# Kernel tuning notes

Hardware: AMD Instinct MI355X
Metric: run time of the kernel (lower is better)

## Reference

```python
import jax, jax.numpy as jnp
import numpy as np

DIM = 256
NH = 8
HGT = 32
WID = 32
B = 8


def rel_indices(S):
    # (1, S*S, S*S, 3) with channels (dx, dy, d^2), matching torch construction
    ind = jnp.arange(S)[None, :] - jnp.arange(S)[:, None]          # (S,S)
    indx = jnp.tile(ind, (S, S))                                    # (S^2,S^2)
    indy = jnp.repeat(jnp.repeat(ind, S, axis=0), S, axis=1)        # (S^2,S^2)
    indd = indx ** 2 + indy ** 2
    return jnp.stack([indx, indy, indd], axis=-1).astype(jnp.float32)[None]


def setup_inputs() -> dict:
    key = jax.random.key(0)
    ks = jax.random.split(key, 8)
    std = 0.02
    x = jax.random.normal(ks[0], (B, DIM, HGT, WID), dtype=jnp.float32)
    input_mask = jnp.ones((B, HGT, WID), dtype=jnp.float32)
    Wqk = jax.random.normal(ks[1], (2 * DIM, DIM), dtype=jnp.float32) * std  # qkv_bias=False
    Wv = jax.random.normal(ks[2], (DIM, DIM), dtype=jnp.float32) * std
    Wproj = jax.random.normal(ks[3], (DIM, DIM), dtype=jnp.float32) * std
    bproj = jnp.zeros((DIM,), dtype=jnp.float32)
    Wpos = jax.random.normal(ks[4], (NH, 3), dtype=jnp.float32) * std
    bpos = jnp.zeros((NH,), dtype=jnp.float32)
    gating = jnp.ones((NH,), dtype=jnp.float32)
    return {"x": x, "input_mask": input_mask, "Wqk": Wqk, "Wv": Wv,
            "Wproj": Wproj, "bproj": bproj, "Wpos": Wpos, "bpos": bpos,
            "gating": gating}


def gpsa_forward(x, input_mask, Wqk, Wv, Wproj, bproj, Wpos, bpos, gating):
    Bq, C, H, W = x.shape
    N = H * W
    nh = gating.shape[0]
    hd = C // nh
    scale = hd ** (-0.5)

    xf = x.reshape(Bq, C, N).transpose(0, 2, 1)          # (B,N,C)
    m = input_mask.reshape(Bq, N)                        # (B,N)

    qk = (xf @ Wqk.T).reshape(Bq, N, 2, nh, hd)
    q = qk[:, :, 0].transpose(0, 2, 1, 3)                # (B,nh,N,hd)
    k = qk[:, :, 1].transpose(0, 2, 1, 3)

    patch_score = jax.nn.softmax(
        jnp.einsum('bhnd,bhmd->bhnm', q, k) * scale, axis=-1)

    rel = rel_indices(H)                                  # (1,N,N,3)
    pos_score = jnp.einsum('unmt,ht->uhnm', rel, Wpos) + bpos[None, :, None, None]
    pos_score = jax.nn.softmax(pos_score, axis=-1)        # (1,nh,N,N)

    g = jax.nn.sigmoid(gating)[None, :, None, None]
    attn = (1.0 - g) * patch_score + g * pos_score
    attn = attn / attn.sum(axis=-1, keepdims=True)
    attn = attn * m[:, None, None, :]                     # mask keys
    attn = attn / attn.sum(axis=-1, keepdims=True)

    v = (xf @ Wv.T).reshape(Bq, N, nh, hd).transpose(0, 2, 1, 3)  # (B,nh,N,hd)
    out = jnp.einsum('bhnm,bhmd->bhnd', attn, v)          # (B,nh,N,hd)
    out = out.transpose(0, 2, 1, 3).reshape(Bq, N, C)
    out = out @ Wproj.T + bproj
    return out.transpose(0, 2, 1).reshape(Bq, C, H, W)


def reference(x, input_mask, Wqk, Wv, Wproj, bproj, Wpos, bpos, gating):
    return gpsa_forward(x, input_mask, Wqk, Wv, Wproj, bproj, Wpos, bpos, gating)
```

## Files before the change

kernel.cpp:

```cpp
#include <hip/hip_runtime.h>
#include <hip/hip_bf16.h>
#include <math.h>

#define B_ 8
#define C_ 256
#define N_ 1024
#define NH_ 8
#define HD_ 32

typedef __attribute__((ext_vector_type(8))) short bf16x8;
typedef __attribute__((ext_vector_type(4))) short bf16x4;
typedef __attribute__((ext_vector_type(4))) float f32x4;
typedef __attribute__((ext_vector_type(16))) float f32x16;
typedef __attribute__((ext_vector_type(2))) unsigned int u32x2;
typedef __attribute__((ext_vector_type(4))) unsigned int u32x4;
#define MFMA16(a,b,c) __builtin_amdgcn_mfma_f32_16x16x32_bf16((a),(b),(c),0,0,0)
#define MFMA32(a,b,c) __builtin_amdgcn_mfma_f32_32x32x16_bf16((a),(b),(c),0,0,0)

static __device__ __forceinline__ short f2bf(float f) {
    __hip_bfloat16 h = __float2bfloat16(f);
    return *reinterpret_cast<short*>(&h);
}
static __device__ __forceinline__ unsigned int cvtpk(float a, float b) {
    unsigned int r;
    asm("v_cvt_pk_bf16_f32 %0, %1, %2" : "=v"(r) : "v"(a), "v"(b));
    return r;
}

#define FS 0.2550352584f

static constexpr size_t OFF_VB   = 0;
static constexpr size_t OFF_QBF  = 8388608;
static constexpr size_t OFF_KFR  = 12582912;
static constexpr size_t OFF_VFR  = 16777216;
static constexpr size_t OFF_E1   = 20971520;
static constexpr size_t OFF_E2   = 21004288;
static constexpr size_t OFF_SE1  = 21037056;
static constexpr size_t OFF_SE2  = 21038080;
static constexpr size_t OFF_A2   = 21039104;
static constexpr size_t A2S      = 36;
static constexpr size_t OFF_O    = 30476288;
static constexpr size_t OFF_WBF  = 34670592;
static constexpr size_t OFF_WPBF = 35063808;
static constexpr size_t OFF_ZFR  = 35194880;

__global__ __launch_bounds__(256) void k_prep(
    const float* __restrict__ Wqk, const float* __restrict__ Wv,
    const float* __restrict__ Wp, const float* __restrict__ mask,
    const float* __restrict__ Wpos, const float* __restrict__ bpos,
    const float* __restrict__ x,
    __hip_bfloat16* __restrict__ wfm, __hip_bfloat16* __restrict__ wpfm,
    __hip_bfloat16* __restrict__ zfrag, __hip_bfloat16* __restrict__ xfm,
    float* __restrict__ e1, float* __restrict__ e2,
    float* __restrict__ se1, float* __restrict__ se2)
{
    const int bx = blockIdx.x;
    const int tid = threadIdx.x;
    __shared__ float ps[2][32][8];
    __shared__ float tile[64][68];
    if (bx < 256) {
        int idx = bx * 256 + tid;
        int row = idx >> 6;
        int c4  = (idx & 63) * 4;
        const float* src = (row < 512) ? (Wqk + (size_t)row*256)
                         : (row < 768) ? (Wv + (size_t)(row-512)*256)
                                       : (Wp + (size_t)(row-768)*256);
        float4 v = *(const float4*)(src + c4);
        bf16x4 pk;
        pk[0] = f2bf(v.x); pk[1] = f2bf(v.y); pk[2] = f2bf(v.z); pk[3] = f2bf(v.w);
        int r2 = (row < 768) ? row : (row - 768);
        __hip_bfloat16* dst = (row < 768) ? wfm : wpfm;
        size_t addr = (size_t)(r2 >> 4)*4096 + (size_t)(c4 >> 5)*512
                    + (size_t)((((c4 >> 3) & 3)*16) + (r2 & 15))*8 + (c4 & 7);
        *(bf16x4*)(dst + addr) = pk;
    } else if (bx < 384) {
        int idx = (bx - 256) * 256 + tid;
        int L8  = idx & 127;
        int mt  = (idx >> 7) & 31;
        int b   = idx >> 12;
        int region = L8 >> 6;
        int slot   = L8 & 63;
        int zrow = slot & 31, shi = slot >> 5;
        bf16x8 v;
        if (zrow == 0) {
            int m = mt*32 + region*16 + shi*8;
            const float* mp = mask + (size_t)b*N_ + m;
            #pragma unroll
            for (int j = 0; j < 8; ++j) v[j] = f2bf(mp[j]);
        } else {
            short c = (zrow == 1) ? (short)0x3F80 : (short)0;
            #pragma unroll
            for (int j = 0; j < 8; ++j) v[j] = c;
        }
        *(bf16x8*)(zfrag + ((size_t)b*32 + mt)*1024 + region*512 + slot*8) = v;
    } else if (bx < 392) {
        const int h = bx - 384;
        const int i = tid >> 3, j4 = (tid & 7) * 4;
        const float wx = Wpos[h*3+0], wy = Wpos[h*3+1], wd = Wpos[h*3+2], bp = bpos[h];
        float fmx = -1e30f, gmx = -1e30f;
        for (int jp = 0; jp < 32; ++jp) {
            float dx = (float)(jp - i);
            float q2 = wd*dx*dx;
            fmx = fmaxf(fmx, wx*dx + q2 + bp);
            gmx = fmaxf(gmx, wy*dx + q2);
        }
        float s1 = 0.f, s2 = 0.f;
        #pragma unroll
        for (int jj = 0; jj < 4; ++jj) {
            int j = j4 + jj;
            float dx = (float)(j - i);
            float q2 = wd*dx*dx;
            float fv = __expf(wx*dx + q2 + bp - fmx);
            float gv = __expf(wy*dx + q2 - gmx);
            e1[h*1024 + i*32 + j] = fv;
            e2[h*1024 + i*32 + j] = gv;
            s1 += fv; s2 += gv;
        }
        ps[0][i][tid & 7] = s1;
        ps[1][i][tid & 7] = s2;
        __syncthreads();
        if (tid < 32) {
            float a = 0.f, c = 0.f;
            #pragma unroll
            for (int k = 0; k < 8; ++k) { a += ps[0][tid][k]; c += ps[1][tid][k]; }
            se1[h*32 + tid] = a;
            se2[h*32 + tid] = c;
        }
    } else {
        const int bx2 = bx - 392;
        const int n0 = (bx2 & 15) * 64, c0 = ((bx2 >> 4) & 3) * 64, b = bx2 >> 6;
        {
            int cl = tid >> 2, nq = (tid & 3) * 16;
            const float* src = x + ((size_t)b*C_ + c0 + cl)*N_ + n0 + nq;
            #pragma unroll
            for (int i = 0; i < 4; ++i)
                *(float4*)&tile[cl][nq + i*4] = ((const float4*)src)[i];
        }
        __syncthreads();
        {
            int nl = tid >> 2, cq = (tid & 3) * 16;
            short pk[16];
            #pragma unroll
            for (int i = 0; i < 16; ++i) pk[i] = f2bf(tile[cq + i][nl]);
            int cg = c0 + cq;
            int ks = cg >> 5, g0 = (cg >> 3) & 3;
            size_t base = ((size_t)b*64 + (n0 >> 4) + (nl >> 4))*4096
                        + (size_t)ks*512 + (size_t)(g0*16 + (nl & 15))*8;
            *(uint4*)(xfm + base)       = *(uint4*)&pk[0];
            *(uint4*)(xfm + base + 128) = *(uint4*)&pk[8];
        }
    }
}

__global__ __launch_bounds__(256) void k_qkv_mfma(
    const __hip_bfloat16* __restrict__ xfm, const __hip_bfloat16* __restrict__ wfm,
    const float* __restrict__ mask,
    __hip_bfloat16* __restrict__ qbf, __hip_bfloat16* __restrict__ kfrag,
    __hip_bfloat16* __restrict__ vfrag, float* __restrict__ vbuf)
{
    const int t = threadIdx.x, w = t >> 6, L = t & 63, lo = L & 15, g = L >> 4;
    const int jw = blockIdx.x * 64 + w * 16;
    const int n0 = blockIdx.y * 64, b = blockIdx.z;

    const __hip_bfloat16* afm = wfm + (size_t)(jw >> 4)*4096 + (size_t)L*8;
    bf16x8 af[8];
    #pragma unroll
    for (int ks = 0; ks < 8; ++ks) af[ks] = *(const bf16x8*)(afm + ks*512);

    const f32x4 Z = {0.f,0.f,0.f,0.f};
    f32x4 D0 = Z, D1 = Z, D2 = Z, D3 = Z;
    const __hip_bfloat16* xb = xfm + ((size_t)b*64 + (n0 >> 4))*4096 + (size_t)L*8;
    #pragma unroll
    for (int ks = 0; ks < 8; ++ks) {
        bf16x8 b0 = *(const bf16x8*)(xb + ks*512);
        bf16x8 b1 = *(const bf16x8*)(xb + 4096 + ks*512);
        bf16x8 b2 = *(const bf16x8*)(xb + 8192 + ks*512);
        bf16x8 b3 = *(const bf16x8*)(xb + 12288 + ks*512);
        D0 = MFMA16(af[ks], b0, D0);
        D1 = MFMA16(af[ks], b1, D1);
        D2 = MFMA16(af[ks], b2, D2);
        D3 = MFMA16(af[ks], b3, D3);
    }
    f32x4 D[4] = {D0, D1, D2, D3};

    const size_t bb = (size_t)b*NH_;
    if (jw < 256) {
        int h = jw >> 5, d0 = (jw & 31) + 4*g;
        #pragma unroll
        for (int nt = 0; nt < 4; ++nt) {
            int nn = n0 + nt*16 + lo;
            bf16x4 pk;
            #pragma unroll
            for (int r = 0; r < 4; ++r) pk[r] = f2bf(D[nt][r] * FS);
            *(bf16x4*)(qbf + ((bb + h)*N_ + nn)*HD_ + d0) = pk;
        }
    } else if (jw < 512) {
        int j2 = jw & 255, h = j2 >> 5, d0 = (j2 & 31) + 4*g;
        size_t base = (bb + h)*32768 + (size_t)(d0 >> 4)*512
                    + (size_t)((d0 >> 3) & 1)*256 + (d0 & 7);
        #pragma unroll
        for (int nt = 0; nt < 4; ++nt) {
            int nn = n0 + nt*16 + lo;
            bf16x4 pk;
            #pragma unroll
            for (int r = 0; r < 4; ++r) pk[r] = f2bf(D[nt][r]);
            *(bf16x4*)(kfrag + base + (size_t)(nn >> 5)*1024 + (nn & 31)*8) = pk;
        }
    } else {
        int j2 = jw - 512, h = j2 >> 5, d0 = (j2 & 31) + 4*g;
        #pragma unroll
        for (int nt = 0; nt < 4; ++nt) {
            int nn = n0 + nt*16 + lo;
            float mval = mask[(size_t)b*N_ + nn];
            float4 fv = make_float4(D[nt][0], D[nt][1], D[nt][2], D[nt][3]);
            *(float4*)(vbuf + ((bb + h)*N_ + nn)*HD_ + d0) = fv;
            size_t vbase = (bb + h)*32768 + (size_t)(nn >> 5)*1024
                         + (size_t)((nn >> 4) & 1)*512 + (size_t)((nn >> 3) & 1)*256
                         + (nn & 7);
            #pragma unroll
            for (int r = 0; r < 4; ++r)
                vfrag[vbase + (size_t)(d0 + r)*8] = __float2bfloat16(D[nt][r] * mval);
        }
    }
}

__global__ __launch_bounds__(256) void k_pos_apply(
    const float* __restrict__ vb, const float* __restrict__ mask,
    const float* __restrict__ e1, const float* __restrict__ e2,
    float* __restrict__ a2)
{
    const int rn = blockIdx.x, h = blockIdx.y, b = blockIdx.z;
    const int tid = threadIdx.x;
    const int cm = tid >> 3, dq = tid & 7;
    __shared__ float t1[32][36];
    __shared__ float e1s[32][36];
    __shared__ float t1m[32];
    __shared__ float e2s[32];
    const float* vbh = vb + (((size_t)b*NH_ + h)*N_)*HD_;
    const float* mb  = mask + (size_t)b*N_;

    {
        int r = tid >> 3, c4 = (tid & 7) * 4;
        *(float4*)&e1s[r][c4] = *(const float4*)(e1 + h*1024 + r*32 + c4);
        if (tid < 32) e2s[tid] = e2[h*1024 + rn*32 + tid];
    }
    __syncthreads();

    {
        float4 acc = make_float4(0.f,0.f,0.f,0.f);
        const float* vcol = vbh + cm*HD_ + dq*4;
        #pragma unroll 8
        for (int rm = 0; rm < 32; ++rm) {
            float4 vv = *(const float4*)(vcol + (size_t)rm*32*HD_);
            float wgt = e2s[rm];
            acc.x = fmaf(wgt, vv.x, acc.x);
            acc.y = fmaf(wgt, vv.y, acc.y);
            acc.z = fmaf(wgt, vv.z, acc.z);
            acc.w = fmaf(wgt, vv.w, acc.w);
        }
        *(float4*)&t1[cm][dq*4] = acc;
    }
    if (tid < 32) {
        float s = 0.f;
        for (int rm = 0; rm < 32; ++rm)
            s = fmaf(e2s[rm], mb[rm*32 + tid], s);
        t1m[tid] = s;
    }
    __syncthreads();

    const size_t bh = (size_t)b*NH_ + h;
    {
        const int cn = cm;
        float4 acc = make_float4(0.f,0.f,0.f,0.f);
        #pragma unroll 8
        for (int ci = 0; ci < 32; ++ci) {
            float wgt = e1s[cn][ci];
            float4 tv = *(const float4*)&t1[ci][dq*4];
            acc.x = fmaf(wgt, tv.x, acc.x);
            acc.y = fmaf(wgt, tv.y, acc.y);
            acc.z = fmaf(wgt, tv.z, acc.z);
            acc.w = fmaf(wgt, tv.w, acc.w);
        }
        int n = rn*32 + cn;
        *(float4*)(a2 + (bh*N_ + n)*A2S + dq*4) = acc;
    }
    if (tid < 32) {
        float s = 0.f;
        for (int ci = 0; ci < 32; ++ci)
            s = fmaf(e1s[tid][ci], t1m[ci], s);
        a2[(bh*N_ + rn*32 + tid)*A2S + 32] = s;
    }
}

__global__ __launch_bounds__(512, 4) void k_attn_mfma(
    const __hip_bfloat16* __restrict__ qbf, const __hip_bfloat16* __restrict__ kfrag,
    const __hip_bfloat16* __restrict__ vfrag, const __hip_bfloat16* __restrict__ zfrag,
    const float* __restrict__ a2, const float* __restrict__ se1,
    const float* __restrict__ se2, const float* __restrict__ gating,
    __hip_bfloat16* __restrict__ ob)
{
    const int bid = blockIdx.x;
    const int swz = ((bid & 7) << 6) | (bid >> 3);
    const int xt = swz & 7, h = (swz >> 3) & 7, b = swz >> 6;

    const int t = threadIdx.x, w = t >> 6, L = t & 63;
    const int ln = L & 31, hi = L >> 5;
    const int nh = w & 3, sp = w >> 2;
    const int n0 = xt * 128 + nh * 32;
    const size_t bh = (size_t)b*NH_ + h;
    const __hip_bfloat16* qh = qbf + bh*(size_t)N_*HD_;
    const size_t spo = (size_t)sp * 16 * 1024;
    const __hip_bfloat16* kf = kfrag + bh*32768 + spo + (size_t)L*8;
    const __hip_bfloat16* vf = vfrag + bh*32768 + spo + (size_t)L*8;
    const __hip_bfloat16* zf = zfrag + (size_t)b*32768 + spo + (size_t)L*8;

    __shared__ float ldsO[128*32];
    __shared__ float ldsZ[128*2];

    bf16x8 qf0 = *(const bf16x8*)(qh + (size_t)(n0 + ln)*HD_ + 8*hi);
    bf16x8 qf1 = *(const bf16x8*)(qh + (size_t)(n0 + ln)*HD_ + 16 + 8*hi);

    f32x16 O; f32x16 Zc;
    #pragma unroll
    for (int i = 0; i < 16; ++i) { O[i] = 0.f; Zc[i] = 0.f; }

    bf16x8 ka0 = *(const bf16x8*)(kf);
    bf16x8 ka1 = *(const bf16x8*)(kf + 512);
    bf16x8 vf0 = *(const bf16x8*)(vf);
    bf16x8 vf1 = *(const bf16x8*)(vf + 512);
    bf16x8 zf0 = *(const bf16x8*)(zf);
    bf16x8 zf1 = *(const bf16x8*)(zf + 512);

    for (int mt = 0; mt < 16; ++mt) {
        f32x16 S;
        #pragma unroll
        for (int i = 0; i < 16; ++i) S[i] = 0.f;
        S = MFMA32(ka0, qf0, S);
        S = MFMA32(ka1, qf1, S);

        const size_t o1 = (size_t)(mt < 15 ? mt + 1 : mt) * 1024;
        bf16x8 nka0 = *(const bf16x8*)(kf + o1);
        bf16x8 nka1 = *(const bf16x8*)(kf + o1 + 512);
        bf16x8 nvf0 = *(const bf16x8*)(vf + o1);
        bf16x8 nvf1 = *(const bf16x8*)(vf + o1 + 512);
        bf16x8 nzf0 = *(const bf16x8*)(zf + o1);
        bf16x8 nzf1 = *(const bf16x8*)(zf + o1 + 512);

        float e[16];
        #pragma unroll
        for (int i = 0; i < 16; ++i) e[i] = exp2f(S[i]);

        unsigned int x01 = cvtpk(e[0], e[1]), x23 = cvtpk(e[2], e[3]);
        unsigned int x45 = cvtpk(e[4], e[5]), x67 = cvtpk(e[6], e[7]);
        u32x2 r02 = __builtin_amdgcn_permlane32_swap(x01, x45, false, false);
        u32x2 r13 = __builtin_amdgcn_permlane32_swap(x23, x67, false, false);
        u32x4 p0u = { r02[0], r13[0], r02[1], r13[1] };
        bf16x8 pa0 = *reinterpret_cast<bf16x8*>(&p0u);
        unsigned int y01 = cvtpk(e[8], e[9]),  y23 = cvtpk(e[10], e[11]);
        unsigned int y45 = cvtpk(e[12], e[13]), y67 = cvtpk(e[14], e[15]);
        u32x2 s02 = __builtin_amdgcn_permlane32_swap(y01, y45, false, false);
        u32x2 s13 = __builtin_amdgcn_permlane32_swap(y23, y67, false, false);
        u32x4 p1u = { s02[0], s13[0], s02[1], s13[1] };
        bf16x8 pa1 = *reinterpret_cast<bf16x8*>(&p1u);

        O  = MFMA32(pa0, vf0, O);
        O  = MFMA32(pa1, vf1, O);
        Zc = MFMA32(pa0, zf0, Zc);
        Zc = MFMA32(pa1, zf1, Zc);

        ka0 = nka0; ka1 = nka1; vf0 = nvf0; vf1 = nvf1; zf0 = nzf0; zf1 = nzf1;
    }

    if (sp == 1) {
        #pragma unroll
        for (int r = 0; r < 16; ++r) {
            int nl = nh*32 + (r&3) + 8*(r>>2) + 4*hi;
            ldsO[nl*32 + ln] = O[r];
        }
        if (ln < 2) {
            #pragma unroll
            for (int r = 0; r < 16; ++r) {
                int nl = nh*32 + (r&3) + 8*(r>>2) + 4*hi;
                ldsZ[nl*2 + ln] = Zc[r];
            }
        }
    }
    __syncthreads();
    if (sp == 0) {
        #pragma unroll
        for (int r = 0; r < 16; ++r) {
            int nl = nh*32 + (r&3) + 8*(r>>2) + 4*hi;
            O[r] += ldsO[nl*32 + ln];
            if (ln < 2) Zc[r] += ldsZ[nl*2 + ln];
        }

        const float gs = 1.f / (1.f + __expf(-gating[h]));
        #pragma unroll
        for (int r = 0; r < 16; ++r) {
            const int n = n0 + (r&3) + 8*(r>>2) + 4*hi;
            float z1m = __shfl(Zc[r], (L & 32) | 0);
            float zsv = __shfl(Zc[r], (L & 32) | 1);
            const float* a2p = a2 + (bh*N_ + n)*A2S;
            float z2m = a2p[32];
            float zp  = se1[h*32 + (n & 31)] * se2[h*32 + (n >> 5)];
            float w1  = (1.f - gs) / zsv;
            float w2  = gs / zp;
            float inv = 1.f / (w1*z1m + w2*z2m);
            float o = (w1*O[r] + w2*a2p[ln]) * inv;
            size_t oaddr = ((size_t)b*64 + (n >> 4))*4096 + (size_t)h*512
                         + (size_t)((ln >> 3)*16 + (n & 15))*8 + (ln & 7);
            ob[oaddr] = __float2bfloat16(o);
        }
    }
}

__global__ __launch_bounds__(256) void k_proj_mfma(
    const __hip_bfloat16* __restrict__ obf, const __hip_bfloat16* __restrict__ wpfm,
    const float* __restrict__ bp, float* __restrict__ out)
{
    const int t = threadIdx.x, w = t >> 6, L = t & 63, lo = L & 15, g = L >> 4;
    const int cw = blockIdx.x * 64 + w * 16;
    const int n0 = blockIdx.y * 64, b = blockIdx.z;

    const __hip_bfloat16* afm = wpfm + (size_t)(cw >> 4)*4096 + (size_t)L*8;
    bf16x8 af[8];
    #pragma unroll
    for (int ks = 0; ks < 8; ++ks) af[ks] = *(const bf16x8*)(afm + ks*512);

    const f32x4 Z = {0.f,0.f,0.f,0.f};
    f32x4 D0 = Z, D1 = Z, D2 = Z, D3 = Z;
    const __hip_bfloat16* xb = obf + ((size_t)b*64 + (n0 >> 4))*4096 + (size_t)L*8;
    #pragma unroll
    for (int ks = 0; ks < 8; ++ks) {
        bf16x8 b0 = *(const bf16x8*)(xb + ks*512);
        bf16x8 b1 = *(const bf16x8*)(xb + 4096 + ks*512);
        bf16x8 b2 = *(const bf16x8*)(xb + 8192 + ks*512);
        bf16x8 b3 = *(const bf16x8*)(xb + 12288 + ks*512);
        D0 = MFMA16(af[ks], b0, D0);
        D1 = MFMA16(af[ks], b1, D1);
        D2 = MFMA16(af[ks], b2, D2);
        D3 = MFMA16(af[ks], b3, D3);
    }
    f32x4 D[4] = {D0, D1, D2, D3};

    float bias[4];
    #pragma unroll
    for (int r = 0; r < 4; ++r) bias[r] = bp[cw + 4*g + r];
    #pragma unroll
    for (int nt = 0; nt < 4; ++nt) {
        int nn = n0 + nt*16 + lo;
        #pragma unroll
        for (int r = 0; r < 4; ++r)
            out[((size_t)b*C_ + cw + 4*g + r)*N_ + nn] = D[nt][r] + bias[r];
    }
}

extern "C" void kernel_launch(void* const* d_in, const int* in_sizes, int n_in,
                              void* d_out, int out_size, void* d_ws, size_t ws_size,
                              hipStream_t stream)
{
    (void)in_sizes; (void)n_in; (void)out_size; (void)ws_size;
    const float* x      = (const float*)d_in[0];
    const float* mask   = (const float*)d_in[1];
    const float* Wqk    = (const float*)d_in[2];
    const float* Wv     = (const float*)d_in[3];
    const float* Wproj  = (const float*)d_in[4];
    const float* bproj  = (const float*)d_in[5];
    const float* Wpos   = (const float*)d_in[6];
    const float* bpos   = (const float*)d_in[7];
    const float* gating = (const float*)d_in[8];
    float* out = (float*)d_out;
    char* w = (char*)d_ws;

    float*          vbuf  = (float*)(w + OFF_VB);
    __hip_bfloat16* qbf   = (__hip_bfloat16*)(w + OFF_QBF);
    __hip_bfloat16* kfrag = (__hip_bfloat16*)(w + OFF_KFR);
    __hip_bfloat16* vfrag = (__hip_bfloat16*)(w + OFF_VFR);
    float*          e1    = (float*)(w + OFF_E1);
    float*          e2    = (float*)(w + OFF_E2);
    float*          se1   = (float*)(w + OFF_SE1);
    float*          se2   = (float*)(w + OFF_SE2);
    float*          a2    = (float*)(w + OFF_A2);
    __hip_bfloat16* obf   = (__hip_bfloat16*)(w + OFF_O);
    __hip_bfloat16* xfm   = (__hip_bfloat16*)(w + OFF_O);
    __hip_bfloat16* wfm   = (__hip_bfloat16*)(w + OFF_WBF);
    __hip_bfloat16* wpfm  = (__hip_bfloat16*)(w + OFF_WPBF);
    __hip_bfloat16* zfrag = (__hip_bfloat16*)(w + OFF_ZFR);

    k_prep<<<dim3(904), dim3(256), 0, stream>>>(Wqk, Wv, Wproj, mask, Wpos, bpos, x,
                                                wfm, wpfm, zfrag, xfm, e1, e2, se1, se2);
    k_qkv_mfma<<<dim3(12,16,8), dim3(256), 0, stream>>>(xfm, wfm, mask, qbf, kfrag, vfrag, vbuf);
    k_pos_apply<<<dim3(32,8,8), dim3(256), 0, stream>>>(vbuf, mask, e1, e2, a2);
    k_attn_mfma<<<dim3(512), dim3(512), 0, stream>>>(qbf, kfrag, vfrag, zfrag, a2, se1, se2, gating, obf);
    k_proj_mfma<<<dim3(4,16,8), dim3(256), 0, stream>>>(obf, wpfm, bproj, out);
}
```

Baseline: 76.91 us.

## Replace mask/sum MFMA with VALU row reductions and double-buffer K/V prefetch

The attention loop no longer uses two extra MFMAs against a padded mask/ones fragment to compute the masked and unmasked row sums of exp scores. Those sums are now accumulated per lane with VALU adds and FMAs, using a compact reordered bf16 mask buffer, then combined across half-waves with shuffles. The loop is also unrolled by two with K/V prefetch two tiles ahead. This cuts MFMA work and the zfrag bandwidth, and the k_prep launch becomes smaller. In exchange it adds VALU work and register pressure per step.

New measurement: 78.99 us. 2.7% more time.

```diff
diff --git a/kernel.cpp b/kernel.cpp
--- a/kernel.cpp
+++ b/kernel.cpp
@@ -20,6 +20,10 @@
 static __device__ __forceinline__ short f2bf(float f) {
     __hip_bfloat16 h = __float2bfloat16(f);
     return *reinterpret_cast<short*>(&h);
+}
+static __device__ __forceinline__ float bf2f(short s) {
+    unsigned int u = ((unsigned int)(unsigned short)s) << 16;
+    return *reinterpret_cast<float*>(&u);
 }
 static __device__ __forceinline__ unsigned int cvtpk(float a, float b) {
     unsigned int r;
@@ -42,7 +46,7 @@
 static constexpr size_t OFF_O    = 30476288;
 static constexpr size_t OFF_WBF  = 34670592;
 static constexpr size_t OFF_WPBF = 35063808;
-static constexpr size_t OFF_ZFR  = 35194880;
+static constexpr size_t OFF_MR   = 35194880;
 
 __global__ __launch_bounds__(256) void k_prep(
     const float* __restrict__ Wqk, const float* __restrict__ Wv,
@@ -50,7 +54,7 @@
     const float* __restrict__ Wpos, const float* __restrict__ bpos,
     const float* __restrict__ x,
     __hip_bfloat16* __restrict__ wfm, __hip_bfloat16* __restrict__ wpfm,
-    __hip_bfloat16* __restrict__ zfrag, __hip_bfloat16* __restrict__ xfm,
+    __hip_bfloat16* __restrict__ maskr, __hip_bfloat16* __restrict__ xfm,
     float* __restrict__ e1, float* __restrict__ e2,
     float* __restrict__ se1, float* __restrict__ se2)
 {
@@ -73,28 +77,8 @@
         size_t addr = (size_t)(r2 >> 4)*4096 + (size_t)(c4 >> 5)*512
                     + (size_t)((((c4 >> 3) & 3)*16) + (r2 & 15))*8 + (c4 & 7);
         *(bf16x4*)(dst + addr) = pk;
-    } else if (bx < 384) {
-        int idx = (bx - 256) * 256 + tid;
-        int L8  = idx & 127;
-        int mt  = (idx >> 7) & 31;
-        int b   = idx >> 12;
-        int region = L8 >> 6;
-        int slot   = L8 & 63;
-        int zrow = slot & 31, shi = slot >> 5;
-        bf16x8 v;
-        if (zrow == 0) {
-            int m = mt*32 + region*16 + shi*8;
-            const float* mp = mask + (size_t)b*N_ + m;
-            #pragma unroll
-            for (int j = 0; j < 8; ++j) v[j] = f2bf(mp[j]);
-        } else {
-            short c = (zrow == 1) ? (short)0x3F80 : (short)0;
-            #pragma unroll
-            for (int j = 0; j < 8; ++j) v[j] = c;
-        }
-        *(bf16x8*)(zfrag + ((size_t)b*32 + mt)*1024 + region*512 + slot*8) = v;
-    } else if (bx < 392) {
-        const int h = bx - 384;
+    } else if (bx < 264) {
+        const int h = bx - 256;
         const int i = tid >> 3, j4 = (tid & 7) * 4;
         const float wx = Wpos[h*3+0], wy = Wpos[h*3+1], wd = Wpos[h*3+2], bp = bpos[h];
         float fmx = -1e30f, gmx = -1e30f;
@@ -126,8 +110,8 @@
             se1[h*32 + tid] = a;
             se2[h*32 + tid] = c;
         }
-    } else {
-        const int bx2 = bx - 392;
+    } else if (bx < 776) {
+        const int bx2 = bx - 264;
         const int n0 = (bx2 & 15) * 64, c0 = ((bx2 >> 4) & 3) * 64, b = bx2 >> 6;
         {
             int cl = tid >> 2, nq = (tid & 3) * 16;
@@ -148,6 +132,19 @@
                         + (size_t)ks*512 + (size_t)(g0*16 + (nl & 15))*8;
             *(uint4*)(xfm + base)       = *(uint4*)&pk[0];
             *(uint4*)(xfm + base + 128) = *(uint4*)&pk[8];
+        }
+    } else {
+        int idx = (bx - 776) * 256 + tid;
+        if (idx < 512) {
+            int b = idx >> 6, mt = (idx >> 1) & 31, hi = idx & 1;
+            const float* mp = mask + (size_t)b*N_ + mt*32 + 4*hi;
+            bf16x8 v0, v1;
+            #pragma unroll
+            for (int i = 0; i < 8; ++i) v0[i] = f2bf(mp[(i&3) + 8*(i>>2)]);
+            #pragma unroll
+            for (int i = 0; i < 8; ++i) { int r = i + 8; v1[i] = f2bf(mp[(r&3) + 8*(r>>2)]); }
+            *(bf16x8*)(maskr + (size_t)idx*16)     = v0;
+            *(bf16x8*)(maskr + (size_t)idx*16 + 8) = v1;
         }
     }
 }
@@ -294,7 +291,7 @@
 
 __global__ __launch_bounds__(512, 4) void k_attn_mfma(
     const __hip_bfloat16* __restrict__ qbf, const __hip_bfloat16* __restrict__ kfrag,
-    const __hip_bfloat16* __restrict__ vfrag, const __hip_bfloat16* __restrict__ zfrag,
+    const __hip_bfloat16* __restrict__ vfrag, const __hip_bfloat16* __restrict__ maskr,
     const float* __restrict__ a2, const float* __restrict__ se1,
     const float* __restrict__ se2, const float* __restrict__ gating,
     __hip_bfloat16* __restrict__ ob)
@@ -312,7 +309,7 @@
     const size_t spo = (size_t)sp * 16 * 1024;
     const __hip_bfloat16* kf = kfrag + bh*32768 + spo + (size_t)L*8;
     const __hip_bfloat16* vf = vfrag + bh*32768 + spo + (size_t)L*8;
-    const __hip_bfloat16* zf = zfrag + (size_t)b*32768 + spo + (size_t)L*8;
+    const __hip_bfloat16* mrp = maskr + ((size_t)(b*32 + sp*16)*2 + hi)*16;
 
     __shared__ float ldsO[128*32];
     __shared__ float ldsZ[128*2];
@@ -320,56 +317,67 @@
     bf16x8 qf0 = *(const bf16x8*)(qh + (size_t)(n0 + ln)*HD_ + 8*hi);
     bf16x8 qf1 = *(const bf16x8*)(qh + (size_t)(n0 + ln)*HD_ + 16 + 8*hi);
 
-    f32x16 O; f32x16 Zc;
-    #pragma unroll
-    for (int i = 0; i < 16; ++i) { O[i] = 0.f; Zc[i] = 0.f; }
-
-    bf16x8 ka0 = *(const bf16x8*)(kf);
-    bf16x8 ka1 = *(const bf16x8*)(kf + 512);
-    bf16x8 vf0 = *(const bf16x8*)(vf);
-    bf16x8 vf1 = *(const bf16x8*)(vf + 512);
-    bf16x8 zf0 = *(const bf16x8*)(zf);
-    bf16x8 zf1 = *(const bf16x8*)(zf + 512);
-
-    for (int mt = 0; mt < 16; ++mt) {
-        f32x16 S;
-        #pragma unroll
-        for (int i = 0; i < 16; ++i) S[i] = 0.f;
-        S = MFMA32(ka0, qf0, S);
-        S = MFMA32(ka1, qf1, S);
-
-        const size_t o1 = (size_t)(mt < 15 ? mt + 1 : mt) * 1024;
-        bf16x8 nka0 = *(const bf16x8*)(kf + o1);
-        bf16x8 nka1 = *(const bf16x8*)(kf + o1 + 512);
-        bf16x8 nvf0 = *(const bf16x8*)(vf + o1);
-        bf16x8 nvf1 = *(const bf16x8*)(vf + o1 + 512);
-        bf16x8 nzf0 = *(const bf16x8*)(zf + o1);
-        bf16x8 nzf1 = *(const bf16x8*)(zf + o1 + 512);
-
-        float e[16];
-        #pragma unroll
-        for (int i = 0; i < 16; ++i) e[i] = exp2f(S[i]);
-
-        unsigned int x01 = cvtpk(e[0], e[1]), x23 = cvtpk(e[2], e[3]);
-        unsigned int x45 = cvtpk(e[4], e[5]), x67 = cvtpk(e[6], e[7]);
-        u32x2 r02 = __builtin_amdgcn_permlane32_swap(x01, x45, false, false);
-        u32x2 r13 = __builtin_amdgcn_permlane32_swap(x23, x67, false, false);
-        u32x4 p0u = { r02[0], r13[0], r02[1], r13[1] };
-        bf16x8 pa0 = *reinterpret_cast<bf16x8*>(&p0u);
-        unsigned int y01 = cvtpk(e[8], e[9]),  y23 = cvtpk(e[10], e[11]);
-        unsigned int y45 = cvtpk(e[12], e[13]), y67 = cvtpk(e[14], e[15]);
-        u32x2 s02 = __builtin_amdgcn_permlane32_swap(y01, y45, false, false);
-        u32x2 s13 = __builtin_amdgcn_permlane32_swap(y23, y67, false, false);
-        u32x4 p1u = { s02[0], s13[0], s02[1], s13[1] };
-        bf16x8 pa1 = *reinterpret_cast<bf16x8*>(&p1u);
-
-        O  = MFMA32(pa0, vf0, O);
-        O  = MFMA32(pa1, vf1, O);
-        Zc = MFMA32(pa0, zf0, Zc);
-        Zc = MFMA32(pa1, zf1, Zc);
-
-        ka0 = nka0; ka1 = nka1; vf0 = nvf0; vf1 = nvf1; zf0 = nzf0; zf1 = nzf1;
-    }
+    f32x16 O;
+    #pragma unroll
+    for (int i = 0; i < 16; ++i) O[i] = 0.f;
+    float zs = 0.f, z1 = 0.f;
+
+    bf16x8 ak0 = *(const bf16x8*)(kf);
+    bf16x8 ak1 = *(const bf16x8*)(kf + 512);
+    bf16x8 av0 = *(const bf16x8*)(vf);
+    bf16x8 av1 = *(const bf16x8*)(vf + 512);
+    bf16x8 bk0 = *(const bf16x8*)(kf + 1024);
+    bf16x8 bk1 = *(const bf16x8*)(kf + 1024 + 512);
+    bf16x8 bv0 = *(const bf16x8*)(vf + 1024);
+    bf16x8 bv1 = *(const bf16x8*)(vf + 1024 + 512);
+
+#define ATTN_STEP(K0,K1,V0,V1,MT_) do {                                        \
+    f32x16 S;                                                                  \
+    _Pragma("unroll")                                                          \
+    for (int i = 0; i < 16; ++i) S[i] = 0.f;                                   \
+    S = MFMA32(K0, qf0, S);                                                    \
+    S = MFMA32(K1, qf1, S);                                                    \
+    const int mtpf = ((MT_) + 2 < 16) ? (MT_) + 2 : 15;                        \
+    const size_t opf = (size_t)mtpf * 1024;                                    \
+    bf16x8 nk0 = *(const bf16x8*)(kf + opf);                                   \
+    bf16x8 nk1 = *(const bf16x8*)(kf + opf + 512);                             \
+    bf16x8 nv0 = *(const bf16x8*)(vf + opf);                                   \
+    bf16x8 nv1 = *(const bf16x8*)(vf + opf + 512);                             \
+    bf16x8 mr0 = *(const bf16x8*)(mrp + (MT_)*32);                             \
+    bf16x8 mr1 = *(const bf16x8*)(mrp + (MT_)*32 + 8);                         \
+    float e[16];                                                               \
+    _Pragma("unroll")                                                          \
+    for (int i = 0; i < 16; ++i) e[i] = exp2f(S[i]);                           \
+    _Pragma("unroll")                                                          \
+    for (int j = 0; j < 8; ++j) {                                              \
+        zs += e[j] + e[8+j];                                                   \
+        z1 = fmaf(e[j], bf2f(mr0[j]), fmaf(e[8+j], bf2f(mr1[j]), z1));         \
+    }                                                                          \
+    unsigned int x01 = cvtpk(e[0], e[1]), x23 = cvtpk(e[2], e[3]);             \
+    unsigned int x45 = cvtpk(e[4], e[5]), x67 = cvtpk(e[6], e[7]);             \
+    u32x2 r02 = __builtin_amdgcn_permlane32_swap(x01, x45, false, false);      \
+    u32x2 r13 = __builtin_amdgcn_permlane32_swap(x23, x67, false, false);      \
+    u32x4 p0u = { r02[0], r13[0], r02[1], r13[1] };                            \
+    bf16x8 pa0 = *reinterpret_cast<bf16x8*>(&p0u);                             \
+    unsigned int y01 = cvtpk(e[8], e[9]),  y23 = cvtpk(e[10], e[11]);          \
+    unsigned int y45 = cvtpk(e[12], e[13]), y67 = cvtpk(e[14], e[15]);         \
+    u32x2 s02 = __builtin_amdgcn_permlane32_swap(y01, y45, false, false);      \
+    u32x2 s13 = __builtin_amdgcn_permlane32_swap(y23, y67, false, false);      \
+    u32x4 p1u = { s02[0], s13[0], s02[1], s13[1] };                            \
+    bf16x8 pa1 = *reinterpret_cast<bf16x8*>(&p1u);                             \
+    O = MFMA32(pa0, V0, O);                                                    \
+    O = MFMA32(pa1, V1, O);                                                    \
+    K0 = nk0; K1 = nk1; V0 = nv0; V1 = nv1;                                    \
+} while (0)
+
+    for (int mt = 0; mt < 16; mt += 2) {
+        ATTN_STEP(ak0, ak1, av0, av1, mt);
+        ATTN_STEP(bk0, bk1, bv0, bv1, mt + 1);
+    }
+#undef ATTN_STEP
+
+    zs += __shfl_xor(zs, 32);
+    z1 += __shfl_xor(z1, 32);
 
     if (sp == 1) {
         #pragma unroll
@@ -377,12 +385,9 @@
             int nl = nh*32 + (r&3) + 8*(r>>2) + 4*hi;
             ldsO[nl*32 + ln] = O[r];
         }
-        if (ln < 2) {
-            #pragma unroll
-            for (int r = 0; r < 16; ++r) {
-                int nl = nh*32 + (r&3) + 8*(r>>2) + 4*hi;
-                ldsZ[nl*2 + ln] = Zc[r];
-            }
+        if (L < 32) {
+            ldsZ[(nh*32 + ln)*2 + 0] = zs;
+            ldsZ[(nh*32 + ln)*2 + 1] = z1;
         }
     }
     __syncthreads();
@@ -391,21 +396,25 @@
         for (int r = 0; r < 16; ++r) {
             int nl = nh*32 + (r&3) + 8*(r>>2) + 4*hi;
             O[r] += ldsO[nl*32 + ln];
-            if (ln < 2) Zc[r] += ldsZ[nl*2 + ln];
+        }
+        if (L < 32) {
+            zs += ldsZ[(nh*32 + ln)*2 + 0];
+            z1 += ldsZ[(nh*32 + ln)*2 + 1];
         }
 
         const float gs = 1.f / (1.f + __expf(-gating[h]));
         #pragma unroll
         for (int r = 0; r < 16; ++r) {
-            const int n = n0 + (r&3) + 8*(r>>2) + 4*hi;
-            float z1m = __shfl(Zc[r], (L & 32) | 0);
-            float zsv = __shfl(Zc[r], (L & 32) | 1);
+            const int crow = (r&3) + 8*(r>>2) + 4*hi;
+            const int n = n0 + crow;
+            float zsv = __shfl(zs, crow);
+            float z1v = __shfl(z1, crow);
             const float* a2p = a2 + (bh*N_ + n)*A2S;
             float z2m = a2p[32];
             float zp  = se1[h*32 + (n & 31)] * se2[h*32 + (n >> 5)];
             float w1  = (1.f - gs) / zsv;
             float w2  = gs / zp;
-            float inv = 1.f / (w1*z1m + w2*z2m);
+            float inv = 1.f / (w1*z1v + w2*z2m);
             float o = (w1*O[r] + w2*a2p[ln]) * inv;
             size_t oaddr = ((size_t)b*64 + (n >> 4))*4096 + (size_t)h*512
                          + (size_t)((ln >> 3)*16 + (n & 15))*8 + (ln & 7);
@@ -485,12 +494,12 @@
     __hip_bfloat16* xfm   = (__hip_bfloat16*)(w + OFF_O);
     __hip_bfloat16* wfm   = (__hip_bfloat16*)(w + OFF_WBF);
     __hip_bfloat16* wpfm  = (__hip_bfloat16*)(w + OFF_WPBF);
-    __hip_bfloat16* zfrag = (__hip_bfloat16*)(w + OFF_ZFR);
-
-    k_prep<<<dim3(904), dim3(256), 0, stream>>>(Wqk, Wv, Wproj, mask, Wpos, bpos, x,
-                                                wfm, wpfm, zfrag, xfm, e1, e2, se1, se2);
+    __hip_bfloat16* maskr = (__hip_bfloat16*)(w + OFF_MR);
+
+    k_prep<<<dim3(778), dim3(256), 0, stream>>>(Wqk, Wv, Wproj, mask, Wpos, bpos, x,
+                                                wfm, wpfm, maskr, xfm, e1, e2, se1, se2);
     k_qkv_mfma<<<dim3(12,16,8), dim3(256), 0, stream>>>(xfm, wfm, mask, qbf, kfrag, vfrag, vbuf);
     k_pos_apply<<<dim3(32,8,8), dim3(256), 0, stream>>>(vbuf, mask, e1, e2, a2);
-    k_attn_mfma<<<dim3(512), dim3(512), 0, stream>>>(qbf, kfrag, vfrag, zfrag, a2, se1, se2, gating, obf);
+    k_attn_mfma<<<dim3(512), dim3(512), 0, stream>>>(qbf, kfrag, vfrag, maskr, a2, se1, se2, gating, obf);
     k_proj_mfma<<<dim3(4,16,8), dim3(256), 0, stream>>>(obf, wpfm, bproj, out);
 }
```
